# Performance work log

Measured on AMD Instinct MI355X. Metric: run time of the kernel, lower is better.

Reference implementation:

```python
import jax, jax.numpy as jnp
import numpy as np

B, T, E, DK, H = 8, 2048, 1024, 64, 16  # dk*num_heads == embedding_dim


def setup_inputs() -> dict:
    key = jax.random.key(0)
    kx, kq, kk, kv, kl = jax.random.split(key, 5)
    x = jax.random.normal(kx, (B, T, E), dtype=jnp.float32)
    # zero-pad a random tail of each sequence so the data-derived padding mask
    # in the forward (length = count of nonzero energy[b,0,:]) is exercised
    lengths = jax.random.randint(kl, (B,), T // 2, T + 1)
    valid = (jnp.arange(T)[None, :, None] < lengths[:, None, None]).astype(jnp.float32)
    x = x * valid
    scale = 0.02
    Wq = jax.random.normal(kq, (E, DK * H), dtype=jnp.float32) * scale
    Wk = jax.random.normal(kk, (E, DK * H), dtype=jnp.float32) * scale
    Wv = jax.random.normal(kv, (E, DK * H), dtype=jnp.float32) * scale
    return {"x": x, "Wq": Wq, "Wk": Wk, "Wv": Wv}


def reference(x, Wq, Wk, Wv):
    # Q,K,V: [B, T, DK*H] (heads are fused, matching the source's bmm math)
    Q = jnp.einsum('bte,ed->btd', x, Wq)
    K = jnp.einsum('bte,ed->btd', x, Wk)
    V = jnp.einsum('bte,ed->btd', x, Wv)
    energy = jnp.einsum('btd,bsd->bts', Q, K)  # [B, T, T]
    # vectorized version of the per-batch loop: length from nonzeros of row 0,
    # then mask all key columns >= length with -inf
    lengths = jnp.sum(energy[:, 0, :] != 0, axis=-1)              # [B]
    col_mask = jnp.arange(T)[None, :] >= lengths[:, None]          # [B, T]
    energy = jnp.where(col_mask[:, None, :], -jnp.inf, energy)
    score = jax.nn.softmax(energy / jnp.sqrt(jnp.float32(DK)), axis=-1)
    return jnp.einsum('bts,bsd->btd', score, V)  # [B, T, DK*H]
```

## Files before the change

kernel.cpp:

```cpp
#include <hip/hip_runtime.h>
#include <hip/hip_bf16.h>


typedef unsigned short u16;
typedef __bf16 bf16x8 __attribute__((ext_vector_type(8)));
typedef float f32x4 __attribute__((ext_vector_type(4)));
typedef unsigned short us8 __attribute__((ext_vector_type(8)));

__device__ __forceinline__ u16 f2bf(float f) {
    union { float f; unsigned u; } x; x.f = f;
    unsigned r = x.u + 0x7FFFu + ((x.u >> 16) & 1u);
    return (u16)(r >> 16);
}
__device__ __forceinline__ u16 f2h(float f) {
    union { _Float16 h; u16 u; } c; c.h = (_Float16)f;
    return c.u;
}
__device__ __forceinline__ float h2f(u16 b) {
    union { u16 u; _Float16 h; } c; c.u = b;
    return (float)c.h;
}

__device__ __forceinline__ void gload_lds16(const void* g, void* l) {
    __builtin_amdgcn_global_load_lds(
        (const __attribute__((address_space(1))) unsigned*)g,
        (__attribute__((address_space(3))) unsigned*)l, 16, 0, 0);
}

__device__ __forceinline__ unsigned lds_off(const void* p) {
    return (unsigned)(size_t)(const __attribute__((address_space(3))) char*)p;
}
__device__ __forceinline__ bf16x8 ds_read16(unsigned a) {
    bf16x8 r;
    asm volatile("ds_read_b128 %0, %1" : "=v"(r) : "v"(a));
    return r;
}

__global__ void cast_x(const float* __restrict__ x, u16* __restrict__ o) {
    int i = blockIdx.x * 256 + threadIdx.x;
    float4 v = ((const float4*)x)[i];
    ushort4 u;
    u.x = f2bf(v.x); u.y = f2bf(v.y); u.z = f2bf(v.z); u.w = f2bf(v.w);
    ((ushort4*)o)[i] = u;
}

__global__ void transpose_cast_w(const float* __restrict__ Wq,
                                 const float* __restrict__ Wk,
                                 const float* __restrict__ Wv,
                                 u16* __restrict__ WT) {
    __shared__ float tile[32][33];
    const float* W = (blockIdx.z == 0) ? Wq : (blockIdx.z == 1) ? Wk : Wv;
    u16* T = WT + (size_t)blockIdx.z * 1048576;
    int n0 = blockIdx.x * 32, e0 = blockIdx.y * 32;
    int tx = threadIdx.x, ty = threadIdx.y;
#pragma unroll
    for (int j = 0; j < 4; ++j) {
        int e = ty + j * 8;
        tile[e][tx] = W[(size_t)(e0 + e) * 1024 + (n0 + tx)];
    }
    __syncthreads();
#pragma unroll
    for (int j = 0; j < 4; ++j) {
        int n = ty + j * 8;
        T[(size_t)(n0 + n) * 1024 + (e0 + tx)] = f2bf(tile[tx][n]);
    }
}

__global__ void calc_lengths(const float* __restrict__ x, int* __restrict__ len) {
    int b = blockIdx.x, tid = threadIdx.x;
    int cnt = 0;
    for (int t = tid; t < 2048; t += 256) {
        float4 v = *(const float4*)(x + ((size_t)b * 2048 + t) * 1024);
        cnt += (v.x != 0.f || v.y != 0.f || v.z != 0.f || v.w != 0.f) ? 1 : 0;
    }
#pragma unroll
    for (int off = 32; off; off >>= 1) cnt += __shfl_xor(cnt, off);
    __shared__ int red[4];
    int wid = tid >> 6, lane = tid & 63;
    if (!lane) red[wid] = cnt;
    __syncthreads();
    if (tid == 0) len[b] = red[0] + red[1] + red[2] + red[3];
}


#define SBAR0 __builtin_amdgcn_sched_barrier(0)

#define STAGE_T(KT, BUF) do { \
  _Pragma("unroll") for (int j_ = 0; j_ < 4; ++j_) \
      gload_lds16(A + offA[j_] + (size_t)(KT) * 64, &As[BUF][ldsC[j_]]); \
  _Pragma("unroll") for (int j_ = 0; j_ < 4; ++j_) \
      gload_lds16(B + offB[j_] + (size_t)(KT) * 64, &Bs[BUF][ldsC[j_]]); \
} while (0)

#define LD_A4(AF, MH) do { \
  _Pragma("unroll") for (int mt_ = 0; mt_ < 4; ++mt_) { \
    AF[0][mt_] = ds_read16(rowA[(MH) * 4 + mt_] + ps0); \
    AF[1][mt_] = ds_read16(rowA[(MH) * 4 + mt_] + ps1); \
  } \
} while (0)

#define LD_B2(BF, NH) do { \
  _Pragma("unroll") for (int nt_ = 0; nt_ < 2; ++nt_) { \
    BF[0][nt_] = ds_read16(rowB[(NH) * 2 + nt_] + ps0); \
    BF[1][nt_] = ds_read16(rowB[(NH) * 2 + nt_] + ps1); \
  } \
} while (0)

#define MFMA_QUAD(AF, BF, MH, NH) do { \
  _Pragma("unroll") for (int s_ = 0; s_ < 2; ++s_) \
  _Pragma("unroll") for (int mt_ = 0; mt_ < 4; ++mt_) \
  _Pragma("unroll") for (int nt_ = 0; nt_ < 2; ++nt_) \
    acc[(MH) * 4 + mt_][(NH) * 2 + nt_] = __builtin_amdgcn_mfma_f32_16x16x32_bf16( \
        AF[s_][mt_], BF[s_][nt_], acc[(MH) * 4 + mt_][(NH) * 2 + nt_], 0, 0, 0); \
} while (0)

template <int MODE>
__global__ __launch_bounds__(512, 2)
void gemm_bt(const u16* __restrict__ A, int lda, size_t sA,
             const u16* __restrict__ B, int ldb, size_t sB,
             void* __restrict__ Cv, void* __restrict__ Cv2,
             int ldc, size_t sC, int Kdim, const int* __restrict__ lenp) {
    __shared__ u16 As[2][256 * 64];
    __shared__ u16 Bs[2][256 * 64];
    const int tid = threadIdx.x;
    const int bz  = blockIdx.z;
    A += (size_t)bz * sA;
    B += (size_t)bz * sB;
    const size_t bm = (size_t)blockIdx.x * 256, bn = (size_t)blockIdx.y * 256;

    bool skip = false;
    int kEnd = Kdim;
    if (MODE == 3) {
        int lenz = lenp[bm >> 11];
        skip = ((int)(bm & 2047) >= lenz);
    } else if (MODE == 4) {
        int lenz = lenp[bz];
        if ((int)bn >= lenz) return;
        skip = ((int)bm >= lenz);
    } else if (MODE == 5) {
        int lenz = lenp[bz];
        int r64 = (lenz + 63) & ~63;
        kEnd = r64 < Kdim ? r64 : Kdim;
    }

    const int wid = tid >> 6, lane = tid & 63;
    const int wm = wid >> 2, wn = wid & 3;
    const int q = lane >> 4, r = lane & 15;
    const int arow0 = wm * 128, brow0 = wn * 64;

    size_t offA[4], offB[4]; int ldsC[4];
#pragma unroll
    for (int j = 0; j < 4; ++j) {
        int c = j * 512 + tid;
        int row = c >> 3;
        int c16 = (c & 7) ^ (row & 7);
        offA[j] = (size_t)(bm + row) * lda + c16 * 8;
        offB[j] = (size_t)(bn + row) * ldb + c16 * 8;
        ldsC[j] = c * 8;
    }

    unsigned rowA[8], rowB[4], swz0, swz1;
    {
        unsigned asB = lds_off(&As[0][0]), bsB = lds_off(&Bs[0][0]);
        swz0 = (unsigned)((q ^ (r & 7)) * 16);
        swz1 = (unsigned)(((q + 4) ^ (r & 7)) * 16);
#pragma unroll
        for (int MH = 0; MH < 2; ++MH)
#pragma unroll
            for (int mt = 0; mt < 4; ++mt)
                rowA[MH * 4 + mt] = asB + (unsigned)((arow0 + MH * 64 + mt * 16 + r) * 128);
#pragma unroll
        for (int NH = 0; NH < 2; ++NH)
#pragma unroll
            for (int nt = 0; nt < 2; ++nt)
                rowB[NH * 2 + nt] = bsB + (unsigned)((brow0 + NH * 32 + nt * 16 + r) * 128);
    }

    f32x4 acc[8][4] = {};

    if (!skip) {
        const int NT = kEnd >> 6;
        STAGE_T(0, 0);
        STAGE_T(1, 1);
        asm volatile("s_waitcnt vmcnt(8)" ::: "memory");
        SBAR0; __builtin_amdgcn_s_barrier(); SBAR0;
        for (int t = 0; t < NT; ++t) {
            const int p = t & 1;
            const unsigned ps0 = (unsigned)(p << 15) + swz0;
            const unsigned ps1 = (unsigned)(p << 15) + swz1;
            bf16x8 a[2][4], b0[2][2], b1[2][2];
            LD_B2(b0, 0);
            LD_A4(a, 0);
            LD_B2(b1, 1);
            asm volatile("s_waitcnt lgkmcnt(4)" ::: "memory");
            SBAR0;
            __builtin_amdgcn_s_setprio(1);
            MFMA_QUAD(a, b0, 0, 0);
            __builtin_amdgcn_s_setprio(0);
            SBAR0;
            asm volatile("s_waitcnt lgkmcnt(0)" ::: "memory");
            SBAR0;
            __builtin_amdgcn_s_setprio(1);
            MFMA_QUAD(a, b1, 0, 1);
            __builtin_amdgcn_s_setprio(0);
            SBAR0;
            LD_A4(a, 1);
            asm volatile("s_waitcnt lgkmcnt(0)" ::: "memory");
            SBAR0;
            __builtin_amdgcn_s_setprio(1);
            MFMA_QUAD(a, b1, 1, 1);
            MFMA_QUAD(a, b0, 1, 0);
            __builtin_amdgcn_s_setprio(0);
            SBAR0;
            __builtin_amdgcn_s_barrier();
            SBAR0;
            if (t + 2 < NT) STAGE_T(t + 2, p);
            SBAR0;
            if (t + 2 < NT)      asm volatile("s_waitcnt vmcnt(8)" ::: "memory");
            else if (t + 1 < NT) asm volatile("s_waitcnt vmcnt(0)" ::: "memory");
            __builtin_amdgcn_s_barrier();
            SBAR0;
        }
    }

    if (MODE == 5) {
        float* C = (float*)Cv + (size_t)bz * sC;
#pragma unroll
        for (int am = 0; am < 8; ++am) {
            size_t row = bm + arow0 + (am >> 2) * 64 + (am & 3) * 16 + q * 4;
#pragma unroll
            for (int an = 0; an < 4; ++an) {
                size_t col = bn + brow0 + (an >> 1) * 32 + (an & 1) * 16 + r;
#pragma unroll
                for (int i = 0; i < 4; ++i)
                    C[(row + i) * (size_t)ldc + col] = acc[am][an][i];
            }
        }
    } else if (MODE == 4) {
        u16* C = (u16*)Cv + (size_t)bz * sC;
#pragma unroll
        for (int am = 0; am < 8; ++am) {
            size_t row = bm + arow0 + (am >> 2) * 64 + (am & 3) * 16 + q * 4;
#pragma unroll
            for (int an = 0; an < 4; ++an) {
                size_t col = bn + brow0 + (an >> 1) * 32 + (an & 1) * 16 + r;
#pragma unroll
                for (int i = 0; i < 4; ++i)
                    C[(row + i) * (size_t)ldc + col] = f2h(acc[am][an][i]);
            }
        }
    } else {
        int region = blockIdx.y >> 2;
        if (region < 2) {
            u16* C = (u16*)Cv + (size_t)region * 16777216;
            size_t cb = bn - (size_t)region * 1024;
#pragma unroll
            for (int am = 0; am < 8; ++am) {
                size_t row = bm + arow0 + (am >> 2) * 64 + (am & 3) * 16 + q * 4;
#pragma unroll
                for (int an = 0; an < 4; ++an) {
                    size_t col = cb + brow0 + (an >> 1) * 32 + (an & 1) * 16 + r;
#pragma unroll
                    for (int i = 0; i < 4; ++i)
                        C[(row + i) * 1024 + col] = f2bf(acc[am][an][i]);
                }
            }
        } else {
            u16* Cb = (u16*)Cv2 + (bm >> 11) * (size_t)(1024 * 2048)
                      + (bn - 2048) * 2048 + (bm & 2047);
#pragma unroll
            for (int an = 0; an < 4; ++an) {
                int cI = brow0 + (an >> 1) * 32 + (an & 1) * 16 + r;
#pragma unroll
                for (int am = 0; am < 8; ++am) {
                    int tI = arow0 + (am >> 2) * 64 + (am & 3) * 16 + q * 4;
                    ushort4 o;
                    o.x = f2bf(acc[am][an][0]);
                    o.y = f2bf(acc[am][an][1]);
                    o.z = f2bf(acc[am][an][2]);
                    o.w = f2bf(acc[am][an][3]);
                    *(ushort4*)(Cb + (size_t)cI * 2048 + tI) = o;
                }
            }
        }
    }
}

__global__ void softmax_rows_w(u16* __restrict__ E, const int* __restrict__ lengths) {
    int row  = blockIdx.x * 4 + (threadIdx.x >> 6);
    int lane = threadIdx.x & 63;
    int len  = lengths[row >> 11];
    u16* e = E + (size_t)row * 2048;

    float vals[32];
#pragma unroll
    for (int j = 0; j < 4; ++j) {
        us8 v = ((const us8*)e)[j * 64 + lane];
#pragma unroll
        for (int w = 0; w < 8; ++w) vals[j * 8 + w] = h2f(v[w]);
    }

    float m = -3.4e38f;
#pragma unroll
    for (int j = 0; j < 4; ++j) {
        int base = (j * 64 + lane) * 8;
#pragma unroll
        for (int w = 0; w < 8; ++w)
            if (base + w < len) m = fmaxf(m, vals[j * 8 + w]);
    }
#pragma unroll
    for (int off = 32; off; off >>= 1) m = fmaxf(m, __shfl_xor(m, off));

    const float C = 0.18033688011112042f;
    float p[32]; float s = 0.f;
#pragma unroll
    for (int j = 0; j < 4; ++j) {
        int base = (j * 64 + lane) * 8;
#pragma unroll
        for (int w = 0; w < 8; ++w) {
            float v = (base + w < len) ? exp2f((vals[j * 8 + w] - m) * C) : 0.f;
            p[j * 8 + w] = v;
            s += v;
        }
    }
#pragma unroll
    for (int off = 32; off; off >>= 1) s += __shfl_xor(s, off);
    float rinv = 1.0f / s;

#pragma unroll
    for (int j = 0; j < 4; ++j) {
        us8 o;
#pragma unroll
        for (int w = 0; w < 8; ++w) o[w] = f2bf(p[j * 8 + w] * rinv);
        ((us8*)e)[j * 64 + lane] = o;
    }
}

extern "C" void kernel_launch(void* const* d_in, const int* in_sizes, int n_in,
                              void* d_out, int out_size, void* d_ws, size_t ws_size,
                              hipStream_t stream) {
    const float* x  = (const float*)d_in[0];
    const float* Wq = (const float*)d_in[1];
    const float* Wk = (const float*)d_in[2];
    const float* Wv = (const float*)d_in[3];
    float* out = (float*)d_out;
    char* ws = (char*)d_ws;

    const size_t SB  = 2097152;
    const size_t SBe = 4194304;

    if (ws_size < 140509440ULL) return;
    int* lengths = (int*)ws;
    u16* x16 = (u16*)(ws + 256);
    u16* WT  = (u16*)(ws + 33554688);
    u16* VT  = (u16*)(ws + 39846144);
    u16* E   = (u16*)(ws + 73400576);
    u16* Qb  = (u16*)d_out;
    u16* Kb  = Qb + 16777216;

    cast_x<<<dim3(16384), dim3(256), 0, stream>>>(x, x16);
    transpose_cast_w<<<dim3(32, 32, 3), dim3(32, 8), 0, stream>>>(Wq, Wk, Wv, WT);
    calc_lengths<<<dim3(8), dim3(256), 0, stream>>>(x, lengths);

    gemm_bt<3><<<dim3(64, 12, 1), 512, 0, stream>>>(x16, 1024, 0, WT, 1024, 0,
                                                    Qb, VT, 1024, 0, 1024, lengths);

    gemm_bt<4><<<dim3(8, 8, 8), 512, 0, stream>>>(Qb, 1024, SB, Kb, 1024, SB,
                                                  E, nullptr, 2048, SBe, 1024, lengths);

    softmax_rows_w<<<dim3(4096), dim3(256), 0, stream>>>(E, lengths);

    gemm_bt<5><<<dim3(8, 4, 8), 512, 0, stream>>>(E, 2048, SBe, VT, 2048, SB,
                                                  out, nullptr, 1024, SB, 2048, lengths);
}
```

Before: 389.6 us.

## Interleave quarter-tile global-to-LDS prefetches with MFMA phases in GEMM loop

The GEMM main loop now splits each tile's global-to-LDS load into four quarter stages (two A halves, two B halves) instead of one bulk stage. Each quarter is issued between MFMA phases: the next tile is prefetched piece by piece during the current tile's compute, and half of the tile after that is issued early. This is meant to spread memory traffic across the iteration and hide load latency behind matrix work, rather than bunching all loads at the loop tail. The cost is several extra workgroup barriers per iteration and tighter buffer-reuse ordering.

Result: no change. 382.5 us (-1.8%).

```diff
diff --git a/kernel.cpp b/kernel.cpp
--- a/kernel.cpp
+++ b/kernel.cpp
@@ -84,12 +84,16 @@
 
 
 #define SBAR0 __builtin_amdgcn_sched_barrier(0)
-
-#define STAGE_T(KT, BUF) do { \
-  _Pragma("unroll") for (int j_ = 0; j_ < 4; ++j_) \
-      gload_lds16(A + offA[j_] + (size_t)(KT) * 64, &As[BUF][ldsC[j_]]); \
-  _Pragma("unroll") for (int j_ = 0; j_ < 4; ++j_) \
-      gload_lds16(B + offB[j_] + (size_t)(KT) * 64, &Bs[BUF][ldsC[j_]]); \
+#define BARRIER do { SBAR0; __builtin_amdgcn_s_barrier(); SBAR0; } while (0)
+
+#define STAGE_HALF(KT, H) do { \
+  if ((H) < 2) { \
+    gload_lds16(A + offA[(H)*2]     + (size_t)(KT) * 64, &As[(KT)&1][ldsC[(H)*2]]); \
+    gload_lds16(A + offA[(H)*2 + 1] + (size_t)(KT) * 64, &As[(KT)&1][ldsC[(H)*2 + 1]]); \
+  } else { \
+    gload_lds16(B + offB[((H)-2)*2]     + (size_t)(KT) * 64, &Bs[(KT)&1][ldsC[((H)-2)*2]]); \
+    gload_lds16(B + offB[((H)-2)*2 + 1] + (size_t)(KT) * 64, &Bs[(KT)&1][ldsC[((H)-2)*2 + 1]]); \
+  } \
 } while (0)
 
 #define LD_A4(AF, MH) do { \
@@ -113,6 +117,8 @@
     acc[(MH) * 4 + mt_][(NH) * 2 + nt_] = __builtin_amdgcn_mfma_f32_16x16x32_bf16( \
         AF[s_][mt_], BF[s_][nt_], acc[(MH) * 4 + mt_][(NH) * 2 + nt_], 0, 0, 0); \
 } while (0)
+
+#define WAIT_LGKM0 do { asm volatile("s_waitcnt lgkmcnt(0)" ::: "memory"); SBAR0; } while (0)
 
 template <int MODE>
 __global__ __launch_bounds__(512, 2)
@@ -180,44 +186,48 @@
 
     if (!skip) {
         const int NT = kEnd >> 6;
-        STAGE_T(0, 0);
-        STAGE_T(1, 1);
-        asm volatile("s_waitcnt vmcnt(8)" ::: "memory");
-        SBAR0; __builtin_amdgcn_s_barrier(); SBAR0;
+        STAGE_HALF(0, 0); STAGE_HALF(0, 1); STAGE_HALF(0, 2); STAGE_HALF(0, 3);
+        STAGE_HALF(1, 0);
+        asm volatile("s_waitcnt vmcnt(2)" ::: "memory");
+        BARRIER;
         for (int t = 0; t < NT; ++t) {
             const int p = t & 1;
             const unsigned ps0 = (unsigned)(p << 15) + swz0;
             const unsigned ps1 = (unsigned)(p << 15) + swz1;
             bf16x8 a[2][4], b0[2][2], b1[2][2];
+            LD_A4(a, 0);
             LD_B2(b0, 0);
-            LD_A4(a, 0);
-            LD_B2(b1, 1);
-            asm volatile("s_waitcnt lgkmcnt(4)" ::: "memory");
-            SBAR0;
+            if (t + 1 < NT) STAGE_HALF(t + 1, 1);
+            asm volatile("s_waitcnt lgkmcnt(8)" ::: "memory");
+            BARRIER;
+            WAIT_LGKM0;
             __builtin_amdgcn_s_setprio(1);
             MFMA_QUAD(a, b0, 0, 0);
             __builtin_amdgcn_s_setprio(0);
-            SBAR0;
-            asm volatile("s_waitcnt lgkmcnt(0)" ::: "memory");
-            SBAR0;
+            BARRIER;
+            LD_B2(b1, 1);
+            if (t + 1 < NT) STAGE_HALF(t + 1, 2);
+            BARRIER;
+            WAIT_LGKM0;
             __builtin_amdgcn_s_setprio(1);
             MFMA_QUAD(a, b1, 0, 1);
             __builtin_amdgcn_s_setprio(0);
-            SBAR0;
+            BARRIER;
             LD_A4(a, 1);
-            asm volatile("s_waitcnt lgkmcnt(0)" ::: "memory");
-            SBAR0;
+            if (t + 1 < NT) STAGE_HALF(t + 1, 3);
+            BARRIER;
+            WAIT_LGKM0;
             __builtin_amdgcn_s_setprio(1);
             MFMA_QUAD(a, b1, 1, 1);
+            __builtin_amdgcn_s_setprio(0);
+            BARRIER;
+            if (t + 2 < NT) STAGE_HALF(t + 2, 0);
+            BARRIER;
+            __builtin_amdgcn_s_setprio(1);
             MFMA_QUAD(a, b0, 1, 0);
             __builtin_amdgcn_s_setprio(0);
             SBAR0;
-            __builtin_amdgcn_s_barrier();
-            SBAR0;
-            if (t + 2 < NT) STAGE_T(t + 2, p);
-            SBAR0;
-            if (t + 2 < NT)      asm volatile("s_waitcnt vmcnt(8)" ::: "memory");
-            else if (t + 1 < NT) asm volatile("s_waitcnt vmcnt(0)" ::: "memory");
+            asm volatile("s_waitcnt vmcnt(2)" ::: "memory");
             __builtin_amdgcn_s_barrier();
             SBAR0;
         }
```

## Shrink GEMM tiles to 128x128 with 4 waves and restructure K-loop pipeline

Applied to the files above, without the earlier changes.

Switches the shared bf16 GEMM from 256x256 tiles with 8 waves to 128x128 tiles with 4 waves, each wave computing a 64x64 sub-tile, and rescales the launch grids for all three GEMMs. The inner loop now loads both K-halves up front and issues the next global-to-LDS stage between the two MFMA groups instead of after all compute. Smaller tiles give 4x more blocks for better CU fill and finer-grained skipping of padded regions. The cost is lower arithmetic intensity per block and more global and LDS traffic.

Result: faster. 374.5 us (-3.9%).

```diff
diff --git a/kernel.cpp b/kernel.cpp
--- a/kernel.cpp
+++ b/kernel.cpp
@@ -92,41 +92,35 @@
       gload_lds16(B + offB[j_] + (size_t)(KT) * 64, &Bs[BUF][ldsC[j_]]); \
 } while (0)
 
-#define LD_A4(AF, MH) do { \
-  _Pragma("unroll") for (int mt_ = 0; mt_ < 4; ++mt_) { \
-    AF[0][mt_] = ds_read16(rowA[(MH) * 4 + mt_] + ps0); \
-    AF[1][mt_] = ds_read16(rowA[(MH) * 4 + mt_] + ps1); \
-  } \
+#define LD_A(S) do { \
+  _Pragma("unroll") for (int mt_ = 0; mt_ < 4; ++mt_) \
+    af[S][mt_] = ds_read16(rowA[mt_] + ((S) ? ps1 : ps0)); \
 } while (0)
-
-#define LD_B2(BF, NH) do { \
-  _Pragma("unroll") for (int nt_ = 0; nt_ < 2; ++nt_) { \
-    BF[0][nt_] = ds_read16(rowB[(NH) * 2 + nt_] + ps0); \
-    BF[1][nt_] = ds_read16(rowB[(NH) * 2 + nt_] + ps1); \
-  } \
+#define LD_B(S) do { \
+  _Pragma("unroll") for (int nt_ = 0; nt_ < 4; ++nt_) \
+    bf[S][nt_] = ds_read16(rowB[nt_] + ((S) ? ps1 : ps0)); \
 } while (0)
 
-#define MFMA_QUAD(AF, BF, MH, NH) do { \
-  _Pragma("unroll") for (int s_ = 0; s_ < 2; ++s_) \
+#define MFMA_S(S) do { \
   _Pragma("unroll") for (int mt_ = 0; mt_ < 4; ++mt_) \
-  _Pragma("unroll") for (int nt_ = 0; nt_ < 2; ++nt_) \
-    acc[(MH) * 4 + mt_][(NH) * 2 + nt_] = __builtin_amdgcn_mfma_f32_16x16x32_bf16( \
-        AF[s_][mt_], BF[s_][nt_], acc[(MH) * 4 + mt_][(NH) * 2 + nt_], 0, 0, 0); \
+  _Pragma("unroll") for (int nt_ = 0; nt_ < 4; ++nt_) \
+    acc[mt_][nt_] = __builtin_amdgcn_mfma_f32_16x16x32_bf16( \
+        af[S][mt_], bf[S][nt_], acc[mt_][nt_], 0, 0, 0); \
 } while (0)
 
 template <int MODE>
-__global__ __launch_bounds__(512, 2)
+__global__ __launch_bounds__(256, 2)
 void gemm_bt(const u16* __restrict__ A, int lda, size_t sA,
              const u16* __restrict__ B, int ldb, size_t sB,
              void* __restrict__ Cv, void* __restrict__ Cv2,
              int ldc, size_t sC, int Kdim, const int* __restrict__ lenp) {
-    __shared__ u16 As[2][256 * 64];
-    __shared__ u16 Bs[2][256 * 64];
+    __shared__ u16 As[2][128 * 64];
+    __shared__ u16 Bs[2][128 * 64];
     const int tid = threadIdx.x;
     const int bz  = blockIdx.z;
     A += (size_t)bz * sA;
     B += (size_t)bz * sB;
-    const size_t bm = (size_t)blockIdx.x * 256, bn = (size_t)blockIdx.y * 256;
+    const size_t bm = (size_t)blockIdx.x * 128, bn = (size_t)blockIdx.y * 128;
 
     bool skip = false;
     int kEnd = Kdim;
@@ -144,14 +138,13 @@
     }
 
     const int wid = tid >> 6, lane = tid & 63;
-    const int wm = wid >> 2, wn = wid & 3;
+    const int wm = wid >> 1, wn = wid & 1;
     const int q = lane >> 4, r = lane & 15;
-    const int arow0 = wm * 128, brow0 = wn * 64;
 
     size_t offA[4], offB[4]; int ldsC[4];
 #pragma unroll
     for (int j = 0; j < 4; ++j) {
-        int c = j * 512 + tid;
+        int c = j * 256 + tid;
         int row = c >> 3;
         int c16 = (c & 7) ^ (row & 7);
         offA[j] = (size_t)(bm + row) * lda + c16 * 8;
@@ -159,24 +152,20 @@
         ldsC[j] = c * 8;
     }
 
-    unsigned rowA[8], rowB[4], swz0, swz1;
+    unsigned rowA[4], rowB[4], swz0, swz1;
     {
         unsigned asB = lds_off(&As[0][0]), bsB = lds_off(&Bs[0][0]);
         swz0 = (unsigned)((q ^ (r & 7)) * 16);
         swz1 = (unsigned)(((q + 4) ^ (r & 7)) * 16);
 #pragma unroll
-        for (int MH = 0; MH < 2; ++MH)
-#pragma unroll
-            for (int mt = 0; mt < 4; ++mt)
-                rowA[MH * 4 + mt] = asB + (unsigned)((arow0 + MH * 64 + mt * 16 + r) * 128);
-#pragma unroll
-        for (int NH = 0; NH < 2; ++NH)
-#pragma unroll
-            for (int nt = 0; nt < 2; ++nt)
-                rowB[NH * 2 + nt] = bsB + (unsigned)((brow0 + NH * 32 + nt * 16 + r) * 128);
-    }
-
-    f32x4 acc[8][4] = {};
+        for (int mt = 0; mt < 4; ++mt)
+            rowA[mt] = asB + (unsigned)((wm * 64 + mt * 16 + r) * 128);
+#pragma unroll
+        for (int nt = 0; nt < 4; ++nt)
+            rowB[nt] = bsB + (unsigned)((wn * 64 + nt * 16 + r) * 128);
+    }
+
+    f32x4 acc[4][4] = {};
 
     if (!skip) {
         const int NT = kEnd >> 6;
@@ -186,35 +175,26 @@
         SBAR0; __builtin_amdgcn_s_barrier(); SBAR0;
         for (int t = 0; t < NT; ++t) {
             const int p = t & 1;
-            const unsigned ps0 = (unsigned)(p << 15) + swz0;
-            const unsigned ps1 = (unsigned)(p << 15) + swz1;
-            bf16x8 a[2][4], b0[2][2], b1[2][2];
-            LD_B2(b0, 0);
-            LD_A4(a, 0);
-            LD_B2(b1, 1);
-            asm volatile("s_waitcnt lgkmcnt(4)" ::: "memory");
+            const unsigned ps0 = (unsigned)(p << 14) + swz0;
+            const unsigned ps1 = (unsigned)(p << 14) + swz1;
+            bf16x8 af[2][4], bf[2][4];
+            LD_A(0); LD_B(0);
+            LD_A(1); LD_B(1);
+            asm volatile("s_waitcnt lgkmcnt(8)" ::: "memory");
             SBAR0;
             __builtin_amdgcn_s_setprio(1);
-            MFMA_QUAD(a, b0, 0, 0);
+            MFMA_S(0);
             __builtin_amdgcn_s_setprio(0);
             SBAR0;
             asm volatile("s_waitcnt lgkmcnt(0)" ::: "memory");
             SBAR0;
+            __builtin_amdgcn_s_barrier();
+            SBAR0;
+            if (t + 2 < NT) STAGE_T(t + 2, p);
+            SBAR0;
             __builtin_amdgcn_s_setprio(1);
-            MFMA_QUAD(a, b1, 0, 1);
+            MFMA_S(1);
             __builtin_amdgcn_s_setprio(0);
-            SBAR0;
-            LD_A4(a, 1);
-            asm volatile("s_waitcnt lgkmcnt(0)" ::: "memory");
-            SBAR0;
-            __builtin_amdgcn_s_setprio(1);
-            MFMA_QUAD(a, b1, 1, 1);
-            MFMA_QUAD(a, b0, 1, 0);
-            __builtin_amdgcn_s_setprio(0);
-            SBAR0;
-            __builtin_amdgcn_s_barrier();
-            SBAR0;
-            if (t + 2 < NT) STAGE_T(t + 2, p);
             SBAR0;
             if (t + 2 < NT)      asm volatile("s_waitcnt vmcnt(8)" ::: "memory");
             else if (t + 1 < NT) asm volatile("s_waitcnt vmcnt(0)" ::: "memory");
@@ -226,59 +206,59 @@
     if (MODE == 5) {
         float* C = (float*)Cv + (size_t)bz * sC;
 #pragma unroll
-        for (int am = 0; am < 8; ++am) {
-            size_t row = bm + arow0 + (am >> 2) * 64 + (am & 3) * 16 + q * 4;
-#pragma unroll
-            for (int an = 0; an < 4; ++an) {
-                size_t col = bn + brow0 + (an >> 1) * 32 + (an & 1) * 16 + r;
+        for (int mt = 0; mt < 4; ++mt) {
+            size_t row = bm + wm * 64 + mt * 16 + q * 4;
+#pragma unroll
+            for (int nt = 0; nt < 4; ++nt) {
+                size_t col = bn + wn * 64 + nt * 16 + r;
 #pragma unroll
                 for (int i = 0; i < 4; ++i)
-                    C[(row + i) * (size_t)ldc + col] = acc[am][an][i];
+                    C[(row + i) * (size_t)ldc + col] = acc[mt][nt][i];
             }
         }
     } else if (MODE == 4) {
         u16* C = (u16*)Cv + (size_t)bz * sC;
 #pragma unroll
-        for (int am = 0; am < 8; ++am) {
-            size_t row = bm + arow0 + (am >> 2) * 64 + (am & 3) * 16 + q * 4;
-#pragma unroll
-            for (int an = 0; an < 4; ++an) {
-                size_t col = bn + brow0 + (an >> 1) * 32 + (an & 1) * 16 + r;
+        for (int mt = 0; mt < 4; ++mt) {
+            size_t row = bm + wm * 64 + mt * 16 + q * 4;
+#pragma unroll
+            for (int nt = 0; nt < 4; ++nt) {
+                size_t col = bn + wn * 64 + nt * 16 + r;
 #pragma unroll
                 for (int i = 0; i < 4; ++i)
-                    C[(row + i) * (size_t)ldc + col] = f2h(acc[am][an][i]);
+                    C[(row + i) * (size_t)ldc + col] = f2h(acc[mt][nt][i]);
             }
         }
     } else {
-        int region = blockIdx.y >> 2;
+        int region = blockIdx.y >> 3;
         if (region < 2) {
             u16* C = (u16*)Cv + (size_t)region * 16777216;
             size_t cb = bn - (size_t)region * 1024;
 #pragma unroll
-            for (int am = 0; am < 8; ++am) {
-                size_t row = bm + arow0 + (am >> 2) * 64 + (am & 3) * 16 + q * 4;
-#pragma unroll
-                for (int an = 0; an < 4; ++an) {
-                    size_t col = cb + brow0 + (an >> 1) * 32 + (an & 1) * 16 + r;
+            for (int mt = 0; mt < 4; ++mt) {
+                size_t row = bm + wm * 64 + mt * 16 + q * 4;
+#pragma unroll
+                for (int nt = 0; nt < 4; ++nt) {
+                    size_t col = cb + wn * 64 + nt * 16 + r;
 #pragma unroll
                     for (int i = 0; i < 4; ++i)
-                        C[(row + i) * 1024 + col] = f2bf(acc[am][an][i]);
+                        C[(row + i) * 1024 + col] = f2bf(acc[mt][nt][i]);
                 }
             }
         } else {
             u16* Cb = (u16*)Cv2 + (bm >> 11) * (size_t)(1024 * 2048)
                       + (bn - 2048) * 2048 + (bm & 2047);
 #pragma unroll
-            for (int an = 0; an < 4; ++an) {
-                int cI = brow0 + (an >> 1) * 32 + (an & 1) * 16 + r;
-#pragma unroll
-                for (int am = 0; am < 8; ++am) {
-                    int tI = arow0 + (am >> 2) * 64 + (am & 3) * 16 + q * 4;
+            for (int nt = 0; nt < 4; ++nt) {
+                int cI = wn * 64 + nt * 16 + r;
+#pragma unroll
+                for (int mt = 0; mt < 4; ++mt) {
+                    int tI = wm * 64 + mt * 16 + q * 4;
                     ushort4 o;
-                    o.x = f2bf(acc[am][an][0]);
-                    o.y = f2bf(acc[am][an][1]);
-                    o.z = f2bf(acc[am][an][2]);
-                    o.w = f2bf(acc[am][an][3]);
+                    o.x = f2bf(acc[mt][nt][0]);
+                    o.y = f2bf(acc[mt][nt][1]);
+                    o.z = f2bf(acc[mt][nt][2]);
+                    o.w = f2bf(acc[mt][nt][3]);
                     *(ushort4*)(Cb + (size_t)cI * 2048 + tI) = o;
                 }
             }
@@ -362,14 +342,14 @@
     transpose_cast_w<<<dim3(32, 32, 3), dim3(32, 8), 0, stream>>>(Wq, Wk, Wv, WT);
     calc_lengths<<<dim3(8), dim3(256), 0, stream>>>(x, lengths);
 
-    gemm_bt<3><<<dim3(64, 12, 1), 512, 0, stream>>>(x16, 1024, 0, WT, 1024, 0,
-                                                    Qb, VT, 1024, 0, 1024, lengths);
-
-    gemm_bt<4><<<dim3(8, 8, 8), 512, 0, stream>>>(Qb, 1024, SB, Kb, 1024, SB,
-                                                  E, nullptr, 2048, SBe, 1024, lengths);
+    gemm_bt<3><<<dim3(128, 24, 1), 256, 0, stream>>>(x16, 1024, 0, WT, 1024, 0,
+                                                     Qb, VT, 1024, 0, 1024, lengths);
+
+    gemm_bt<4><<<dim3(16, 16, 8), 256, 0, stream>>>(Qb, 1024, SB, Kb, 1024, SB,
+                                                    E, nullptr, 2048, SBe, 1024, lengths);
 
     softmax_rows_w<<<dim3(4096), dim3(256), 0, stream>>>(E, lengths);
 
-    gemm_bt<5><<<dim3(8, 4, 8), 512, 0, stream>>>(E, 2048, SBe, VT, 2048, SB,
-                                                  out, nullptr, 1024, SB, 2048, lengths);
-}
+    gemm_bt<5><<<dim3(16, 8, 8), 256, 0, stream>>>(E, 2048, SBe, VT, 2048, SB,
+                                                   out, nullptr, 1024, SB, 2048, lengths);
+}
```
